# Optimization experiments

Measured on AMD Instinct MI355X. Metric: run time of the kernel, lower is better.

## Reference

```python
import jax, jax.numpy as jnp
import numpy as np

B, N, C, HF, NUM_CLASS = 2, 500, 512, 25, 20
POOL = 7
STRIDE = 32.0


def setup_inputs() -> dict:
    key = jax.random.key(0)
    ks = jax.random.split(key, 9)
    feature_map = jax.random.normal(ks[0], (B, C, HF, HF), dtype=jnp.float32)
    # Post-NMS boxes (r0, c0, r1, c1) in image coords [0, 800], guaranteed
    # to have floor(r1/32) - floor(r0/32) >= 1 so every crop is non-empty
    # (matches the module's assumption that extract_fature_map is non-empty).
    r0 = jax.random.uniform(ks[1], (B, N), minval=0.0, maxval=700.0)
    c0 = jax.random.uniform(ks[2], (B, N), minval=0.0, maxval=700.0)
    hh = jax.random.uniform(ks[3], (B, N), minval=64.0, maxval=100.0)
    ww = jax.random.uniform(ks[4], (B, N), minval=64.0, maxval=100.0)
    boxes = jnp.stack([r0, c0, jnp.clip(r0 + hh, 0, 800.0), jnp.clip(c0 + ww, 0, 800.0)], axis=-1)
    fc_w = jax.random.normal(ks[5], (4096, POOL * POOL * C), dtype=jnp.float32) * 0.01
    fc_b = jnp.zeros((4096,), dtype=jnp.float32)
    l_w = jax.random.normal(ks[6], (NUM_CLASS * 4, 4096), dtype=jnp.float32) * 0.01
    l_b = jnp.zeros((NUM_CLASS * 4,), dtype=jnp.float32)
    s_w = jax.random.normal(ks[7], (NUM_CLASS + 1, 4096), dtype=jnp.float32) * 0.01
    s_b = jnp.zeros((NUM_CLASS + 1,), dtype=jnp.float32)
    return {"feature_map": feature_map, "boxes": boxes, "fc_w": fc_w, "fc_b": fc_b,
            "l_w": l_w, "l_b": l_b, "s_w": s_w, "s_b": s_b}


def _bin_edges(start, size):
    # Adaptive avg pool bin boundaries: floor(k*size/P), ceil((k+1)*size/P),
    # offset by the crop start. start/size: [B, N] int32. Returns [B, N, P] each.
    k = jnp.arange(POOL, dtype=jnp.int32)
    lo = start[..., None] + (k * size[..., None]) // POOL
    hi = start[..., None] + ((k + 1) * size[..., None] + POOL - 1) // POOL
    return lo, hi


def _roi_pool(feature_map, boxes):
    # Exact equivalent of per-box crop + AdaptiveAvgPool2d((7,7)) via an
    # integral image, fully vectorized over all B*N boxes.
    coords = (boxes / STRIDE).astype(jnp.int32)  # int() cast, coords >= 0
    r0, c0, r1, c1 = coords[..., 0], coords[..., 1], coords[..., 2], coords[..., 3]
    rs, re = _bin_edges(r0, r1 - r0)  # [B, N, 7]
    cs, ce = _bin_edges(c0, c1 - c0)
    # Integral image: I[b, ch, i, j] = sum(fm[b, ch, :i, :j]); shape [B, C, 26, 26]
    I = jnp.pad(feature_map, ((0, 0), (0, 0), (1, 0), (1, 0))).cumsum(2).cumsum(3)

    def pool_one(I_b, rs_b, re_b, cs_b, ce_b):
        def corner(r, c):  # [N,7],[N,7] -> [C, N, 7, 7]
            return I_b[:, r[:, :, None], c[:, None, :]]
        S = corner(re_b, ce_b) - corner(rs_b, ce_b) - corner(re_b, cs_b) + corner(rs_b, cs_b)
        area = ((re_b - rs_b)[:, :, None] * (ce_b - cs_b)[:, None, :]).astype(I_b.dtype)
        return S / area  # [C, N, 7, 7]

    pooled = jax.vmap(pool_one)(I, rs, re, cs, ce)  # [B, C, N, 7, 7]
    # torch.flatten(pool, 0) flattens (C, 7, 7) in C-major order
    return pooled.transpose(0, 2, 1, 3, 4).reshape(B, N, C * POOL * POOL)


def reference(feature_map, boxes, fc_w, fc_b, l_w, l_b, s_w, s_b):
    feat = _roi_pool(feature_map, boxes)                      # [B, N, 25088]
    fc = jnp.einsum('bnk,fk->bnf', feat, fc_w) + fc_b         # [B, N, 4096]
    l_fc = jnp.einsum('bnf,lf->bnl', fc, l_w) + l_b           # [B, N, 80]
    s_fc = jnp.einsum('bnf,sf->bns', fc, s_w) + s_b           # [B, N, 21]
    max_index = jnp.argmax(s_fc, axis=-1)                     # [B, N]
    idx = max_index[..., None] + jnp.arange(4)                # l_fc[mi:mi+4]
    l_out = jnp.take_along_axis(l_fc, idx, axis=-1)           # [B, N, 4]
    return l_out, s_fc
```

## Files before the change

kernel.cpp:

```cpp
#include <hip/hip_runtime.h>

#define BATCH 2
#define NBOX 500
#define CH 512
#define HFD 25
#define IW 26
#define IRC 676
#define IRCP2 768
#define PPOOL 7
#define NP 49
#define NCLS 20
#define NO 101
#define OP2 112
#define MFRAG 7
#define KD 25088
#define FDIM 4096
#define NSTEP_TOT 128
#define FSPLIT 8
#define WCSTEPS 16
#define S_WC ((size_t)KD * OP2)
#define NFRAG_H (NP * 16 * MFRAG)

typedef __attribute__((ext_vector_type(4))) float f32x4;
typedef __attribute__((ext_vector_type(8))) short bf16x8;
typedef __attribute__((ext_vector_type(4))) unsigned int u32v4;

#define MFMA16 __builtin_amdgcn_mfma_f32_16x16x32_bf16

#define SPLIT2PK(V0, V1, HW, MW)                                       \
  {                                                                    \
    unsigned u0_ = __float_as_uint(V0), u1_ = __float_as_uint(V1);     \
    HW = (u0_ >> 16) | (u1_ & 0xffff0000u);                            \
    float r0_ = (V0) - __uint_as_float(u0_ & 0xffff0000u);             \
    float r1_ = (V1) - __uint_as_float(u1_ & 0xffff0000u);             \
    unsigned m0_ = __float_as_uint(r0_), m1_ = __float_as_uint(r1_);   \
    m0_ += 0x7fffu + ((m0_ >> 16) & 1u);                               \
    m1_ += 0x7fffu + ((m1_ >> 16) & 1u);                               \
    MW = (m0_ >> 16) | (m1_ & 0xffff0000u);                            \
  }

#define SPLIT3PK(V0, V1, HW, MW, LW)                                   \
  {                                                                    \
    unsigned u0_ = __float_as_uint(V0), u1_ = __float_as_uint(V1);     \
    HW = (u0_ >> 16) | (u1_ & 0xffff0000u);                            \
    float r0_ = (V0) - __uint_as_float(u0_ & 0xffff0000u);             \
    float r1_ = (V1) - __uint_as_float(u1_ & 0xffff0000u);             \
    unsigned m0_ = __float_as_uint(r0_), m1_ = __float_as_uint(r1_);   \
    MW = (m0_ >> 16) | (m1_ & 0xffff0000u);                            \
    float s0_ = r0_ - __uint_as_float(m0_ & 0xffff0000u);              \
    float s1_ = r1_ - __uint_as_float(m1_ & 0xffff0000u);              \
    LW = (__float_as_uint(s0_) >> 16) |                                \
         (__float_as_uint(s1_) & 0xffff0000u);                         \
  }

__global__ void k_lt(const float* __restrict__ lw, const float* __restrict__ sw,
                     u32v4* __restrict__ Ahi, u32v4* __restrict__ Amd) {
    int t = blockIdx.x * 256 + threadIdx.x;
    if (t >= MFRAG * NSTEP_TOT * 64) return;
    int lane = t & 63;
    int wv = t >> 6;
    int s = wv & 127, mf = wv >> 7;
    int o = mf * 16 + (lane & 15);
    int f0 = s * 32 + (lane >> 4) * 8;
    float v[8];
    const float* row = nullptr;
    if (o < 80) row = lw + (size_t)o * FDIM;
    else if (o < NO) row = sw + (size_t)(o - 80) * FDIM;
    #pragma unroll
    for (int j = 0; j < 8; ++j) v[j] = row ? row[f0 + j] : 0.f;
    u32v4 hw, mw;
    #pragma unroll
    for (int w = 0; w < 4; ++w)
        SPLIT2PK(v[2 * w], v[2 * w + 1], hw[w], mw[w]);
    Ahi[(size_t)wv * 64 + lane] = hw;
    Amd[(size_t)wv * 64 + lane] = mw;
}

__global__ void k_integral(const float* __restrict__ fm, float* __restrict__ I) {
    int gtid = blockIdx.x * blockDim.x + threadIdx.x;
    int wid = gtid >> 6;
    int lane = gtid & 63;
    if (wid >= BATCH * CH) return;
    const float* src = fm + (size_t)wid * (HFD * HFD);
    float* dst = I + (size_t)wid * IRCP2;
    if (lane < IW) dst[lane] = 0.f;
    if (lane >= 1 && lane < IW) dst[lane * IW] = 0.f;
    int c = lane;
    float acc = 0.f;
    for (int r = 0; r < HFD; ++r) {
        float v = (c < HFD) ? src[r * HFD + c] : 0.f;
        #pragma unroll
        for (int d = 1; d < 32; d <<= 1) {
            float t = __shfl_up(v, d, 64);
            if (lane >= d) v += t;
        }
        acc += v;
        if (c < HFD) dst[(r + 1) * IW + (c + 1)] = acc;
    }
}

__global__ void k_bias(const float* __restrict__ lw, const float* __restrict__ sw,
                       const float* __restrict__ fcb, const float* __restrict__ lb,
                       const float* __restrict__ sb, float* __restrict__ bias) {
    int o = blockIdx.x;
    __shared__ float red[256];
    float s = 0.f;
    if (o < NO) {
        const float* row = (o < 80) ? (lw + (size_t)o * FDIM) : (sw + (size_t)(o - 80) * FDIM);
        for (int f = threadIdx.x; f < FDIM; f += 256) s += row[f] * fcb[f];
    }
    red[threadIdx.x] = s;
    __syncthreads();
    for (int st = 128; st > 0; st >>= 1) {
        if ((int)threadIdx.x < st) red[threadIdx.x] += red[threadIdx.x + st];
        __syncthreads();
    }
    if (threadIdx.x == 0) {
        float bv = 0.f;
        if (o < 80) bv = red[0] + lb[o];
        else if (o < NO) bv = red[0] + sb[o - 80];
        bias[o] = bv;
    }
}

#define WC_STEP(CUR, NXT, S)                                                  \
  {                                                                           \
    u32v4 ah[MFRAG], am[MFRAG];                                               \
    _Pragma("unroll")                                                         \
    for (int mf = 0; mf < MFRAG; ++mf) {                                      \
      size_t ai = (size_t)((mf * 128 + fs * WCSTEPS + (S)) * 64 + lane);      \
      ah[mf] = Ahi[ai]; am[mf] = Amd[ai];                                     \
    }                                                                         \
    if ((S) + 1 < WCSTEPS) {                                                  \
      const float* bpn = bp + (size_t)((S) + 1) * 32 * KD;                    \
      _Pragma("unroll")                                                       \
      for (int nf = 0; nf < 2; ++nf)                                          \
        _Pragma("unroll")                                                     \
        for (int j = 0; j < 8; ++j)                                           \
          NXT[nf][j] = bpn[(size_t)j * KD + nf * 16];                         \
    }                                                                         \
    _Pragma("unroll")                                                         \
    for (int nf = 0; nf < 2; ++nf) {                                          \
      u32v4 bhw, bmw;                                                         \
      _Pragma("unroll")                                                       \
      for (int w_ = 0; w_ < 4; ++w_)                                          \
        SPLIT2PK(CUR[nf][2 * w_], CUR[nf][2 * w_ + 1], bhw[w_], bmw[w_]);     \
      bf16x8 bh = __builtin_bit_cast(bf16x8, bhw);                            \
      bf16x8 bm = __builtin_bit_cast(bf16x8, bmw);                            \
      _Pragma("unroll")                                                       \
      for (int mf = 0; mf < MFRAG; ++mf) {                                    \
        bf16x8 a_h = __builtin_bit_cast(bf16x8, ah[mf]);                      \
        bf16x8 a_m = __builtin_bit_cast(bf16x8, am[mf]);                      \
        acc[mf][nf] = MFMA16(a_h, bh, acc[mf][nf], 0, 0, 0);                  \
        acc[mf][nf] = MFMA16(a_m, bh, acc[mf][nf], 0, 0, 0);                  \
        acc[mf][nf] = MFMA16(a_h, bm, acc[mf][nf], 0, 0, 0);                  \
      }                                                                       \
    }                                                                         \
  }

__global__ void __launch_bounds__(256, 3) k_wc(const float* __restrict__ W1,
                                               const u32v4* __restrict__ Ahi,
                                               const u32v4* __restrict__ Amd,
                                               float* __restrict__ Wcp) {
    int lane = threadIdx.x & 63;
    int w = threadIdx.x >> 6;
    int kb = blockIdx.x;
    int fs = blockIdx.y;
    int k0 = kb * 128 + w * 32;
    int row0 = (lane >> 4) * 8;
    int col = lane & 15;
    const float* bp = W1 + (size_t)(fs * 512 + row0) * KD + k0 + col;

    f32x4 acc[MFRAG][2];
    #pragma unroll
    for (int mf = 0; mf < MFRAG; ++mf) {
        acc[mf][0] = (f32x4){0.f, 0.f, 0.f, 0.f};
        acc[mf][1] = (f32x4){0.f, 0.f, 0.f, 0.f};
    }
    float b0[2][8], b1[2][8];
    #pragma unroll
    for (int nf = 0; nf < 2; ++nf)
        #pragma unroll
        for (int j = 0; j < 8; ++j) b0[nf][j] = bp[(size_t)j * KD + nf * 16];

    for (int s = 0; s < WCSTEPS; s += 2) {
        WC_STEP(b0, b1, s);
        WC_STEP(b1, b0, s + 1);
    }

    float* wp = Wcp + (size_t)fs * S_WC;
    #pragma unroll
    for (int mf = 0; mf < MFRAG; ++mf)
        #pragma unroll
        for (int nf = 0; nf < 2; ++nf) {
            size_t k = (size_t)k0 + nf * 16 + col;
            int o = mf * 16 + ((lane >> 4) << 2);
            *(f32x4*)(wp + k * OP2 + o) = acc[mf][nf];
        }
}

__global__ void k_redsplit(const float* __restrict__ Wcp, u32v4* __restrict__ Whi,
                           u32v4* __restrict__ Wmd, u32v4* __restrict__ Wlo) {
    int t = blockIdx.x * 256 + threadIdx.x;
    int lane = t & 63;
    int fi = t >> 6;
    int p = fi / (16 * MFRAG);
    int rem = fi - p * (16 * MFRAG);
    int cs = rem / MFRAG, mf = rem - cs * MFRAG;
    int o = mf * 16 + (lane & 15);
    int c0 = cs * 32 + (lane >> 4) * 8;
    float v[8];
    #pragma unroll
    for (int j = 0; j < 8; ++j) {
        size_t base = ((size_t)(c0 + j) * NP + p) * OP2 + o;
        float s = 0.f;
        #pragma unroll
        for (int i = 0; i < FSPLIT; ++i) s += Wcp[base + (size_t)i * S_WC];
        v[j] = s;
    }
    u32v4 hw, mw, lww;
    #pragma unroll
    for (int w = 0; w < 4; ++w)
        SPLIT3PK(v[2 * w], v[2 * w + 1], hw[w], mw[w], lww[w]);
    Whi[(size_t)fi * 64 + lane] = hw;
    Wmd[(size_t)fi * 64 + lane] = mw;
    Wlo[(size_t)fi * 64 + lane] = lww;
}

#define KH_STEP(CUR, NXT, S)                                                  \
  {                                                                           \
    if ((S) + 1 < 16) {                                                       \
      _Pragma("unroll")                                                       \
      for (int nf = 0; nf < 2; ++nf)                                          \
        _Pragma("unroll")                                                     \
        for (int j = 0; j < 8; ++j)                                           \
          NXT[nf][j] = Ib[(size_t)(((S) + 1) * 32 + rowg * 8 + j) * IRCP2 + nf * 16]; \
    }                                                                         \
    bf16x8 bh[2], bm[2], bl[2];                                               \
    _Pragma("unroll")                                                         \
    for (int nf = 0; nf < 2; ++nf) {                                          \
      u32v4 bhw, bmw, blw;                                                    \
      _Pragma("unroll")                                                       \
      for (int w_ = 0; w_ < 4; ++w_)                                          \
        SPLIT3PK(CUR[nf][2 * w_], CUR[nf][2 * w_ + 1], bhw[w_], bmw[w_], blw[w_]); \
      bh[nf] = __builtin_bit_cast(bf16x8, bhw);                               \
      bm[nf] = __builtin_bit_cast(bf16x8, bmw);                               \
      bl[nf] = __builtin_bit_cast(bf16x8, blw);                               \
    }                                                                         \
    _Pragma("unroll")                                                         \
    for (int mf = 0; mf < MFRAG; ++mf) {                                      \
      size_t ai = (size_t)(((p * 16 + (S)) * MFRAG + mf) * 64 + lane);        \
      bf16x8 a_h = __builtin_bit_cast(bf16x8, Whi[ai]);                       \
      bf16x8 a_m = __builtin_bit_cast(bf16x8, Wmd[ai]);                       \
      bf16x8 a_l = __builtin_bit_cast(bf16x8, Wlo[ai]);                       \
      _Pragma("unroll")                                                       \
      for (int nf = 0; nf < 2; ++nf) {                                        \
        acc[mf][nf] = MFMA16(a_h, bh[nf], acc[mf][nf], 0, 0, 0);              \
        acc[mf][nf] = MFMA16(a_m, bh[nf], acc[mf][nf], 0, 0, 0);              \
        acc[mf][nf] = MFMA16(a_h, bm[nf], acc[mf][nf], 0, 0, 0);              \
        acc[mf][nf] = MFMA16(a_m, bm[nf], acc[mf][nf], 0, 0, 0);              \
        acc[mf][nf] = MFMA16(a_l, bh[nf], acc[mf][nf], 0, 0, 0);              \
        acc[mf][nf] = MFMA16(a_h, bl[nf], acc[mf][nf], 0, 0, 0);              \
      }                                                                       \
    }                                                                         \
  }

__global__ void __launch_bounds__(256, 2) k_h(const float* __restrict__ I,
                                              const u32v4* __restrict__ Whi,
                                              const u32v4* __restrict__ Wmd,
                                              const u32v4* __restrict__ Wlo,
                                              float* __restrict__ H) {
    int lane = threadIdx.x & 63;
    int w = threadIdx.x >> 6;
    int rcb = blockIdx.x, p = blockIdx.y, b = blockIdx.z;
    int col = lane & 15, rowg = lane >> 4;
    int rcw = rcb * 128 + w * 32;
    const float* Ib = I + (size_t)b * CH * IRCP2 + rcw + col;

    f32x4 acc[MFRAG][2];
    #pragma unroll
    for (int mf = 0; mf < MFRAG; ++mf) {
        acc[mf][0] = (f32x4){0.f, 0.f, 0.f, 0.f};
        acc[mf][1] = (f32x4){0.f, 0.f, 0.f, 0.f};
    }
    float ib0[2][8], ib1[2][8];
    #pragma unroll
    for (int nf = 0; nf < 2; ++nf)
        #pragma unroll
        for (int j = 0; j < 8; ++j)
            ib0[nf][j] = Ib[(size_t)(rowg * 8 + j) * IRCP2 + nf * 16];

    for (int s = 0; s < 16; s += 2) {
        KH_STEP(ib0, ib1, s);
        KH_STEP(ib1, ib0, s + 1);
    }

    #pragma unroll
    for (int mf = 0; mf < MFRAG; ++mf)
        #pragma unroll
        for (int nf = 0; nf < 2; ++nf) {
            int rc = rcw + nf * 16 + col;
            if (rc < IRC) {
                float* hp = H + (((size_t)(b * NP + p)) * IRC + rc) * OP2
                            + mf * 16 + rowg * 4;
                *(f32x4*)hp = acc[mf][nf];
            }
        }
}

__global__ void __launch_bounds__(256) k_out(const float* __restrict__ boxes,
                                             const float* __restrict__ H,
                                             const float* __restrict__ bias,
                                             float* __restrict__ out) {
    int n = blockIdx.x, b = blockIdx.y;
    int t = threadIdx.x;
    __shared__ int srs[PPOOL], sre[PPOOL], scs[PPOOL], sce[PPOOL];
    __shared__ float sinv[NP];
    __shared__ float psum[2][NO];
    __shared__ float sl[NO];
    __shared__ int smi;
    const float* bx = boxes + ((size_t)b * NBOX + n) * 4;
    if (t < PPOOL) {
        int r0 = (int)(bx[0] / 32.0f);
        int c0 = (int)(bx[1] / 32.0f);
        int r1 = (int)(bx[2] / 32.0f);
        int c1 = (int)(bx[3] / 32.0f);
        int sr = r1 - r0, sc = c1 - c0;
        srs[t] = r0 + (t * sr) / PPOOL;
        sre[t] = r0 + ((t + 1) * sr + PPOOL - 1) / PPOOL;
        scs[t] = c0 + (t * sc) / PPOOL;
        sce[t] = c0 + ((t + 1) * sc + PPOOL - 1) / PPOOL;
    }
    __syncthreads();
    if (t < NP) {
        int ph = t / PPOOL, pw = t - ph * PPOOL;
        sinv[t] = 1.0f / (float)((sre[ph] - srs[ph]) * (sce[pw] - scs[pw]));
    }
    __syncthreads();
    int o = t & 127, half = t >> 7;
    if (o < NO) {
        int p0 = half * 25, p1 = half ? NP : 25;
        float acc = 0.f;
        const float* Hb = H + (size_t)b * NP * IRC * OP2 + o;
        for (int p = p0; p < p1; ++p) {
            int ph = p / PPOOL, pw = p - ph * PPOOL;
            const float* Hp = Hb + (size_t)p * IRC * OP2;
            int re = sre[ph], rs = srs[ph], ce = sce[pw], cs = scs[pw];
            float v = Hp[(size_t)(re * IW + ce) * OP2] - Hp[(size_t)(rs * IW + ce) * OP2]
                    - Hp[(size_t)(re * IW + cs) * OP2] + Hp[(size_t)(rs * IW + cs) * OP2];
            acc += v * sinv[p];
        }
        psum[half][o] = acc;
    }
    __syncthreads();
    if (t < NO) {
        float v = psum[0][t] + psum[1][t] + bias[t];
        sl[t] = v;
        if (t >= 80)
            out[(size_t)(4 * BATCH * NBOX) + ((size_t)b * NBOX + n) * (NCLS + 1) + (t - 80)] = v;
    }
    __syncthreads();
    if (t == 0) {
        float best = sl[80]; int mi = 0;
        for (int s = 1; s <= NCLS; ++s) {
            float v = sl[80 + s];
            if (v > best) { best = v; mi = s; }
        }
        smi = mi;
    }
    __syncthreads();
    if (t < 4) out[((size_t)b * NBOX + n) * 4 + t] = sl[smi + t];
}

extern "C" void kernel_launch(void* const* d_in, const int* in_sizes, int n_in,
                              void* d_out, int out_size, void* d_ws, size_t ws_size,
                              hipStream_t stream) {
    const float* fm    = (const float*)d_in[0];
    const float* boxes = (const float*)d_in[1];
    const float* fcw   = (const float*)d_in[2];
    const float* fcb   = (const float*)d_in[3];
    const float* lw    = (const float*)d_in[4];
    const float* lb    = (const float*)d_in[5];
    const float* sw    = (const float*)d_in[6];
    const float* sb    = (const float*)d_in[7];
    float* out = (float*)d_out;

    float* ws = (float*)d_ws;
    float* I    = ws;
    u32v4* Ahi  = (u32v4*)(I + (size_t)BATCH * CH * IRCP2);
    u32v4* Amd  = Ahi + MFRAG * NSTEP_TOT * 64;
    float* bias = (float*)(Amd + MFRAG * NSTEP_TOT * 64);
    float* Wcp  = bias + 128;
    u32v4* Whi  = (u32v4*)(Wcp + (size_t)FSPLIT * S_WC);
    u32v4* Wmd  = Whi + (size_t)NFRAG_H * 64;
    u32v4* Wlo  = Wmd + (size_t)NFRAG_H * 64;
    float* H    = (float*)(Wlo + (size_t)NFRAG_H * 64);

    hipLaunchKernelGGL(k_lt, dim3(224), dim3(256), 0, stream, lw, sw, Ahi, Amd);
    hipLaunchKernelGGL(k_integral, dim3(256), dim3(256), 0, stream, fm, I);
    hipLaunchKernelGGL(k_bias, dim3(104), dim3(256), 0, stream, lw, sw, fcb, lb, sb, bias);
    hipLaunchKernelGGL(k_wc, dim3(196, FSPLIT), dim3(256), 0, stream, fcw, Ahi, Amd, Wcp);
    hipLaunchKernelGGL(k_redsplit, dim3(NFRAG_H * 64 / 256), dim3(256), 0, stream, Wcp, Whi, Wmd, Wlo);
    hipLaunchKernelGGL(k_h, dim3(6, NP, BATCH), dim3(256), 0, stream, I, Whi, Wmd, Wlo, H);
    hipLaunchKernelGGL(k_out, dim3(NBOX, BATCH), dim3(256), 0, stream, boxes, H, bias, out);
}
```

Before: 280.5 us.

## Stage W1 tiles in LDS via async global_load_lds with swizzled double buffering

The k_wc kernel used to read W1 straight from global memory with strided per-lane scalar loads held in a register prefetch. It now copies each 32x128 W1 tile into a double-buffered, XOR-swizzled LDS area using global_load_lds 16-byte transfers, then reads B fragments from LDS. The aim is coalesced global access and lower register pressure. The mid-word split also drops its rounding step (truncation instead of round-to-nearest), which trims ALU work but slightly changes numerics. The cost is an added block-wide barrier per step and extra LDS use, which may reduce occupancy.

```diff
diff --git a/kernel.cpp b/kernel.cpp
--- a/kernel.cpp
+++ b/kernel.cpp
@@ -27,6 +27,10 @@
 
 #define MFMA16 __builtin_amdgcn_mfma_f32_16x16x32_bf16
 
+typedef __attribute__((address_space(1))) const unsigned int guint;
+typedef __attribute__((address_space(3))) unsigned int luint;
+#define GLL16(G, L) __builtin_amdgcn_global_load_lds((guint*)(G), (luint*)(L), 16, 0, 0)
+
 #define SPLIT2PK(V0, V1, HW, MW)                                       \
   {                                                                    \
     unsigned u0_ = __float_as_uint(V0), u1_ = __float_as_uint(V1);     \
@@ -37,6 +41,16 @@
     m0_ += 0x7fffu + ((m0_ >> 16) & 1u);                               \
     m1_ += 0x7fffu + ((m1_ >> 16) & 1u);                               \
     MW = (m0_ >> 16) | (m1_ & 0xffff0000u);                            \
+  }
+
+#define SPLIT2T(V0, V1, HW, MW)                                        \
+  {                                                                    \
+    unsigned u0_ = __float_as_uint(V0), u1_ = __float_as_uint(V1);     \
+    HW = (u0_ >> 16) | (u1_ & 0xffff0000u);                            \
+    float r0_ = (V0) - __uint_as_float(u0_ & 0xffff0000u);             \
+    float r1_ = (V1) - __uint_as_float(u1_ & 0xffff0000u);             \
+    MW = (__float_as_uint(r0_) >> 16) |                                \
+         (__float_as_uint(r1_) & 0xffff0000u);                         \
   }
 
 #define SPLIT3PK(V0, V1, HW, MW, LW)                                   \
@@ -123,7 +137,16 @@
     }
 }
 
-#define WC_STEP(CUR, NXT, S)                                                  \
+#define WC_STAGE(S, DB)                                                       \
+  {                                                                           \
+    const float* gs_ = gsrc0 + (size_t)((S) * 32) * KD;                       \
+    float* lb_ = &Bs[DB][w * 1024];                                           \
+    _Pragma("unroll")                                                         \
+    for (int i_ = 0; i_ < 4; ++i_)                                            \
+      GLL16(gs_ + (size_t)(i_ * 2) * KD, lb_ + i_ * 256);                     \
+  }
+
+#define WC_STEP(S, DB)                                                        \
   {                                                                           \
     u32v4 ah[MFRAG], am[MFRAG];                                               \
     _Pragma("unroll")                                                         \
@@ -131,30 +154,33 @@
       size_t ai = (size_t)((mf * 128 + fs * WCSTEPS + (S)) * 64 + lane);      \
       ah[mf] = Ahi[ai]; am[mf] = Amd[ai];                                     \
     }                                                                         \
-    if ((S) + 1 < WCSTEPS) {                                                  \
-      const float* bpn = bp + (size_t)((S) + 1) * 32 * KD;                    \
-      _Pragma("unroll")                                                       \
-      for (int nf = 0; nf < 2; ++nf)                                          \
-        _Pragma("unroll")                                                     \
-        for (int j = 0; j < 8; ++j)                                           \
-          NXT[nf][j] = bpn[(size_t)j * KD + nf * 16];                         \
-    }                                                                         \
-    _Pragma("unroll")                                                         \
-    for (int nf = 0; nf < 2; ++nf) {                                          \
-      u32v4 bhw, bmw;                                                         \
-      _Pragma("unroll")                                                       \
-      for (int w_ = 0; w_ < 4; ++w_)                                          \
-        SPLIT2PK(CUR[nf][2 * w_], CUR[nf][2 * w_ + 1], bhw[w_], bmw[w_]);     \
-      bf16x8 bh = __builtin_bit_cast(bf16x8, bhw);                            \
-      bf16x8 bm = __builtin_bit_cast(bf16x8, bmw);                            \
-      _Pragma("unroll")                                                       \
-      for (int mf = 0; mf < MFRAG; ++mf) {                                    \
-        bf16x8 a_h = __builtin_bit_cast(bf16x8, ah[mf]);                      \
-        bf16x8 a_m = __builtin_bit_cast(bf16x8, am[mf]);                      \
-        acc[mf][nf] = MFMA16(a_h, bh, acc[mf][nf], 0, 0, 0);                  \
-        acc[mf][nf] = MFMA16(a_m, bh, acc[mf][nf], 0, 0, 0);                  \
-        acc[mf][nf] = MFMA16(a_h, bm, acc[mf][nf], 0, 0, 0);                  \
-      }                                                                       \
+    const char* bs_ = (const char*)&Bs[DB][0];                                \
+    float bv0[8], bv1[8];                                                     \
+    _Pragma("unroll")                                                         \
+    for (int j = 0; j < 8; ++j) {                                             \
+      bv0[j] = *(const float*)(bs_ + rb + j * 512 + kb0);                     \
+      bv1[j] = *(const float*)(bs_ + rb + j * 512 + kb1);                     \
+    }                                                                         \
+    u32v4 bh0w, bm0w, bh1w, bm1w;                                             \
+    _Pragma("unroll")                                                         \
+    for (int w_ = 0; w_ < 4; ++w_) {                                          \
+      SPLIT2T(bv0[2 * w_], bv0[2 * w_ + 1], bh0w[w_], bm0w[w_]);              \
+      SPLIT2T(bv1[2 * w_], bv1[2 * w_ + 1], bh1w[w_], bm1w[w_]);              \
+    }                                                                         \
+    bf16x8 bh0 = __builtin_bit_cast(bf16x8, bh0w);                            \
+    bf16x8 bm0 = __builtin_bit_cast(bf16x8, bm0w);                            \
+    bf16x8 bh1 = __builtin_bit_cast(bf16x8, bh1w);                            \
+    bf16x8 bm1 = __builtin_bit_cast(bf16x8, bm1w);                            \
+    _Pragma("unroll")                                                         \
+    for (int mf = 0; mf < MFRAG; ++mf) {                                      \
+      bf16x8 a_h = __builtin_bit_cast(bf16x8, ah[mf]);                        \
+      bf16x8 a_m = __builtin_bit_cast(bf16x8, am[mf]);                        \
+      acc[mf][0] = MFMA16(a_h, bh0, acc[mf][0], 0, 0, 0);                     \
+      acc[mf][0] = MFMA16(a_m, bh0, acc[mf][0], 0, 0, 0);                     \
+      acc[mf][0] = MFMA16(a_h, bm0, acc[mf][0], 0, 0, 0);                     \
+      acc[mf][1] = MFMA16(a_h, bh1, acc[mf][1], 0, 0, 0);                     \
+      acc[mf][1] = MFMA16(a_m, bh1, acc[mf][1], 0, 0, 0);                     \
+      acc[mf][1] = MFMA16(a_h, bm1, acc[mf][1], 0, 0, 0);                     \
     }                                                                         \
   }
 
@@ -162,14 +188,21 @@
                                                const u32v4* __restrict__ Ahi,
                                                const u32v4* __restrict__ Amd,
                                                float* __restrict__ Wcp) {
+    __shared__ float Bs[2][32 * 128];
     int lane = threadIdx.x & 63;
     int w = threadIdx.x >> 6;
     int kb = blockIdx.x;
     int fs = blockIdx.y;
-    int k0 = kb * 128 + w * 32;
-    int row0 = (lane >> 4) * 8;
-    int col = lane & 15;
-    const float* bp = W1 + (size_t)(fs * 512 + row0) * KD + k0 + col;
+    int k0 = kb * 128;
+    int col = lane & 15, rowg = lane >> 4;
+
+    int lin = lane & 31, hi = lane >> 5;
+    int skel = (((lin * 16) ^ ((w & 3) << 5)) >> 2);
+    const float* gsrc0 = W1 + ((size_t)(fs * 512) + w * 8 + hi) * KD + k0 + skel;
+
+    unsigned rb = (unsigned)(rowg * 4096);
+    unsigned kb0 = ((unsigned)((w * 32 + col) * 4)) ^ ((unsigned)rowg << 5);
+    unsigned kb1 = ((unsigned)((w * 32 + col + 16) * 4)) ^ ((unsigned)rowg << 5);
 
     f32x4 acc[MFRAG][2];
     #pragma unroll
@@ -177,15 +210,14 @@
         acc[mf][0] = (f32x4){0.f, 0.f, 0.f, 0.f};
         acc[mf][1] = (f32x4){0.f, 0.f, 0.f, 0.f};
     }
-    float b0[2][8], b1[2][8];
-    #pragma unroll
-    for (int nf = 0; nf < 2; ++nf)
-        #pragma unroll
-        for (int j = 0; j < 8; ++j) b0[nf][j] = bp[(size_t)j * KD + nf * 16];
-
-    for (int s = 0; s < WCSTEPS; s += 2) {
-        WC_STEP(b0, b1, s);
-        WC_STEP(b1, b0, s + 1);
+
+    WC_STAGE(0, 0);
+    __syncthreads();
+    for (int s = 0; s < WCSTEPS; ++s) {
+        int db = s & 1;
+        if (s + 1 < WCSTEPS) WC_STAGE(s + 1, db ^ 1);
+        WC_STEP(s, db);
+        __syncthreads();
     }
 
     float* wp = Wcp + (size_t)fs * S_WC;
@@ -193,8 +225,8 @@
     for (int mf = 0; mf < MFRAG; ++mf)
         #pragma unroll
         for (int nf = 0; nf < 2; ++nf) {
-            size_t k = (size_t)k0 + nf * 16 + col;
-            int o = mf * 16 + ((lane >> 4) << 2);
+            size_t k = (size_t)k0 + w * 32 + nf * 16 + col;
+            int o = mf * 16 + (rowg << 2);
             *(f32x4*)(wp + k * OP2 + o) = acc[mf][nf];
         }
 }
```

Measured after the change: 262.0 us. 1.07x faster.

## Stage fc_w tiles through LDS with async global_load_lds double buffering

Applied to the files above, without the earlier changes.

The k_wc kernel, which folds the 4096x25088 fc weight into the small output projection, now copies fc_w tiles into swizzled shared memory using global_load_lds. The copies are double buffered so the next stage loads while the current one computes. Each block now covers 256 k columns, four fragments per wave, over a grid half as wide. The low bf16 residual is truncated rather than rounded to save ALU work. The aim is to turn strided per-lane global reads of the dominant weight stream into coalesced 16-byte transfers that overlap with MFMA work, at the cost of 64KB of LDS, lower occupancy (launch bounds 2) and a slight precision change.

```diff
diff --git a/kernel.cpp b/kernel.cpp
--- a/kernel.cpp
+++ b/kernel.cpp
@@ -27,6 +27,10 @@
 
 #define MFMA16 __builtin_amdgcn_mfma_f32_16x16x32_bf16
 
+typedef __attribute__((address_space(1))) const unsigned int guint;
+typedef __attribute__((address_space(3))) unsigned int luint;
+#define GLL16(G, L) __builtin_amdgcn_global_load_lds((guint*)(G), (luint*)(L), 16, 0, 0)
+
 #define SPLIT2PK(V0, V1, HW, MW)                                       \
   {                                                                    \
     unsigned u0_ = __float_as_uint(V0), u1_ = __float_as_uint(V1);     \
@@ -37,6 +41,16 @@
     m0_ += 0x7fffu + ((m0_ >> 16) & 1u);                               \
     m1_ += 0x7fffu + ((m1_ >> 16) & 1u);                               \
     MW = (m0_ >> 16) | (m1_ & 0xffff0000u);                            \
+  }
+
+#define SPLIT2T(V0, V1, HW, MW)                                        \
+  {                                                                    \
+    unsigned u0_ = __float_as_uint(V0), u1_ = __float_as_uint(V1);     \
+    HW = (u0_ >> 16) | (u1_ & 0xffff0000u);                            \
+    float r0_ = (V0) - __uint_as_float(u0_ & 0xffff0000u);             \
+    float r1_ = (V1) - __uint_as_float(u1_ & 0xffff0000u);             \
+    MW = (__float_as_uint(r0_) >> 16) |                                \
+         (__float_as_uint(r1_) & 0xffff0000u);                         \
   }
 
 #define SPLIT3PK(V0, V1, HW, MW, LW)                                   \
@@ -123,7 +137,18 @@
     }
 }
 
-#define WC_STEP(CUR, NXT, S)                                                  \
+#define WC_STAGE(S, DB)                                                       \
+  {                                                                           \
+    const float* gb_ = W1 + (size_t)(fs * 512 + (S) * 32 + w) * KD + k0;      \
+    _Pragma("unroll")                                                         \
+    for (int i_ = 0; i_ < 8; ++i_) {                                          \
+      unsigned gc_ = (lb16 ^ ((unsigned)(i_ >> 1) << 6)) >> 2;                \
+      GLL16(gb_ + (size_t)(4 * i_) * KD + gc_,                                \
+            &Bs[DB][i_ * 1024 + w * 256]);                                    \
+    }                                                                         \
+  }
+
+#define WC_STEP(S, DB)                                                        \
   {                                                                           \
     u32v4 ah[MFRAG], am[MFRAG];                                               \
     _Pragma("unroll")                                                         \
@@ -131,20 +156,17 @@
       size_t ai = (size_t)((mf * 128 + fs * WCSTEPS + (S)) * 64 + lane);      \
       ah[mf] = Ahi[ai]; am[mf] = Amd[ai];                                     \
     }                                                                         \
-    if ((S) + 1 < WCSTEPS) {                                                  \
-      const float* bpn = bp + (size_t)((S) + 1) * 32 * KD;                    \
-      _Pragma("unroll")                                                       \
-      for (int nf = 0; nf < 2; ++nf)                                          \
-        _Pragma("unroll")                                                     \
-        for (int j = 0; j < 8; ++j)                                           \
-          NXT[nf][j] = bpn[(size_t)j * KD + nf * 16];                         \
-    }                                                                         \
+    const char* bs_ = (const char*)&Bs[DB][0];                                \
     _Pragma("unroll")                                                         \
-    for (int nf = 0; nf < 2; ++nf) {                                          \
+    for (int nf = 0; nf < 4; ++nf) {                                          \
+      float bv[8];                                                            \
+      _Pragma("unroll")                                                       \
+      for (int j = 0; j < 8; ++j)                                             \
+        bv[j] = *(const float*)(bs_ + (rowg * 8 + j) * 1024 + kb[nf]);        \
       u32v4 bhw, bmw;                                                         \
       _Pragma("unroll")                                                       \
       for (int w_ = 0; w_ < 4; ++w_)                                          \
-        SPLIT2PK(CUR[nf][2 * w_], CUR[nf][2 * w_ + 1], bhw[w_], bmw[w_]);     \
+        SPLIT2T(bv[2 * w_], bv[2 * w_ + 1], bhw[w_], bmw[w_]);                \
       bf16x8 bh = __builtin_bit_cast(bf16x8, bhw);                            \
       bf16x8 bm = __builtin_bit_cast(bf16x8, bmw);                            \
       _Pragma("unroll")                                                       \
@@ -158,43 +180,47 @@
     }                                                                         \
   }
 
-__global__ void __launch_bounds__(256, 3) k_wc(const float* __restrict__ W1,
+__global__ void __launch_bounds__(256, 2) k_wc(const float* __restrict__ W1,
                                                const u32v4* __restrict__ Ahi,
                                                const u32v4* __restrict__ Amd,
                                                float* __restrict__ Wcp) {
+    __shared__ float Bs[2][32 * 256];
     int lane = threadIdx.x & 63;
     int w = threadIdx.x >> 6;
-    int kb = blockIdx.x;
+    int kblk = blockIdx.x;
     int fs = blockIdx.y;
-    int k0 = kb * 128 + w * 32;
-    int row0 = (lane >> 4) * 8;
-    int col = lane & 15;
-    const float* bp = W1 + (size_t)(fs * 512 + row0) * KD + k0 + col;
-
-    f32x4 acc[MFRAG][2];
-    #pragma unroll
-    for (int mf = 0; mf < MFRAG; ++mf) {
-        acc[mf][0] = (f32x4){0.f, 0.f, 0.f, 0.f};
-        acc[mf][1] = (f32x4){0.f, 0.f, 0.f, 0.f};
-    }
-    float b0[2][8], b1[2][8];
-    #pragma unroll
-    for (int nf = 0; nf < 2; ++nf)
-        #pragma unroll
-        for (int j = 0; j < 8; ++j) b0[nf][j] = bp[(size_t)j * KD + nf * 16];
-
-    for (int s = 0; s < WCSTEPS; s += 2) {
-        WC_STEP(b0, b1, s);
-        WC_STEP(b1, b0, s + 1);
+    int k0 = kblk * 256;
+    int col = lane & 15, rowg = lane >> 4;
+    unsigned lb16 = (unsigned)lane * 16;
+
+    unsigned kb[4];
+    #pragma unroll
+    for (int nf = 0; nf < 4; ++nf)
+        kb[nf] = ((unsigned)((w * 64 + nf * 16 + col) * 4)) ^ ((unsigned)rowg << 6);
+
+    f32x4 acc[MFRAG][4];
+    #pragma unroll
+    for (int mf = 0; mf < MFRAG; ++mf)
+        #pragma unroll
+        for (int nf = 0; nf < 4; ++nf)
+            acc[mf][nf] = (f32x4){0.f, 0.f, 0.f, 0.f};
+
+    WC_STAGE(0, 0);
+    __syncthreads();
+    for (int s = 0; s < WCSTEPS; ++s) {
+        int db = s & 1;
+        if (s + 1 < WCSTEPS) WC_STAGE(s + 1, db ^ 1);
+        WC_STEP(s, db);
+        __syncthreads();
     }
 
     float* wp = Wcp + (size_t)fs * S_WC;
     #pragma unroll
     for (int mf = 0; mf < MFRAG; ++mf)
         #pragma unroll
-        for (int nf = 0; nf < 2; ++nf) {
-            size_t k = (size_t)k0 + nf * 16 + col;
-            int o = mf * 16 + ((lane >> 4) << 2);
+        for (int nf = 0; nf < 4; ++nf) {
+            size_t k = (size_t)k0 + w * 64 + nf * 16 + col;
+            int o = mf * 16 + (rowg << 2);
             *(f32x4*)(wp + k * OP2 + o) = acc[mf][nf];
         }
 }
@@ -399,7 +425,7 @@
     hipLaunchKernelGGL(k_lt, dim3(224), dim3(256), 0, stream, lw, sw, Ahi, Amd);
     hipLaunchKernelGGL(k_integral, dim3(256), dim3(256), 0, stream, fm, I);
     hipLaunchKernelGGL(k_bias, dim3(104), dim3(256), 0, stream, lw, sw, fcb, lb, sb, bias);
-    hipLaunchKernelGGL(k_wc, dim3(196, FSPLIT), dim3(256), 0, stream, fcw, Ahi, Amd, Wcp);
+    hipLaunchKernelGGL(k_wc, dim3(98, FSPLIT), dim3(256), 0, stream, fcw, Ahi, Amd, Wcp);
     hipLaunchKernelGGL(k_redsplit, dim3(NFRAG_H * 64 / 256), dim3(256), 0, stream, Wcp, Whi, Wmd, Wlo);
     hipLaunchKernelGGL(k_h, dim3(6, NP, BATCH), dim3(256), 0, stream, I, Whi, Wmd, Wlo, H);
     hipLaunchKernelGGL(k_out, dim3(NBOX, BATCH), dim3(256), 0, stream, boxes, H, bias, out);
```

Result: faster. 250.7 us (-10.6%).
